# Optimization experiments

Hardware: AMD Instinct MI355X
Metric: run time of the kernel (lower is better)

## Reference

```python
import jax, jax.numpy as jnp
import numpy as np

N, M, D_IN, HID = 6144, 6144, 16, 256
TEMP = 0.1


def setup_inputs() -> dict:
    key = jax.random.key(0)
    ks = jax.random.split(key, 6)
    sc = lambda k, shape, s: jax.random.normal(k, shape, jnp.float32) * s
    return {
        "q_multivectors": jax.random.normal(ks[0], (N, D_IN), jnp.float32),
        "ret_multivectors": jax.random.normal(ks[1], (M, D_IN), jnp.float32),
        # compressor: LazyLinear(D_IN->HID), GELU, Linear(HID->HID)
        "W1": sc(ks[2], (HID, D_IN), 0.1), "b1": jnp.zeros((HID,), jnp.float32),
        "W2": sc(ks[3], (HID, HID), 0.05), "b2": jnp.zeros((HID,), jnp.float32),
        # nn.Bilinear(HID, HID, 1): weight [1,HID,HID] -> [HID,HID], bias [1] -> scalar
        "Wb": sc(ks[4], (HID, HID), 0.02), "b_bil": jnp.zeros((), jnp.float32),
        "slack_q": jnp.zeros((1,), jnp.float32),
        "slack_ret": jnp.zeros((1,), jnp.float32),
    }


def reference(q_multivectors, ret_multivectors, W1, b1, W2, b2, Wb, b_bil, slack_q, slack_ret):
    def compress(x):  # Linear -> exact GELU -> Linear
        return jax.nn.gelu(x @ W1.T + b1, approximate=False) @ W2.T + b2

    h_q = compress(q_multivectors)    # [n, H]
    h_r = compress(ret_multivectors)  # [m, H]

    # Bilinear(h_q_i, h_r_j) as low-rank factorization: (h_q @ Wb) @ h_r^T + bias
    logits = (h_q @ Wb) @ h_r.T + b_bil  # [n, m]
    n, m = logits.shape

    # row softmax with slack column, then drop slack
    with_slack_col = jnp.concatenate([logits, jnp.broadcast_to(slack_q, (n, 1))], axis=1)
    pi_rows = jax.nn.softmax(with_slack_col / TEMP, axis=1)[:, :-1]

    # column softmax with slack row, then drop slack
    with_slack_row = jnp.concatenate([logits, jnp.broadcast_to(slack_ret, (1, m))], axis=0)
    pi_cols = jax.nn.softmax(with_slack_row / TEMP, axis=0)[:-1, :]

    pi_approx = 0.5 * (pi_rows + pi_cols)
    return pi_approx, logits
```

## Files before the change

kernel.cpp:

```cpp
#include <hip/hip_runtime.h>
#include <hip/hip_bf16.h>
#include <math.h>

#define NQ 6144
#define MR 6144
#define DIN 16
#define HID 256
#define INV_T 10.0f

typedef __attribute__((ext_vector_type(4))) float f32x4;
typedef __attribute__((ext_vector_type(8))) short bf16x8;


static __device__ __forceinline__ unsigned short f2bf(float f) {
  __hip_bfloat16 h = __float2bfloat16(f);
  return __builtin_bit_cast(unsigned short, h);
}

static __device__ __forceinline__ void gload16(const void* g, void* l) {
  __builtin_amdgcn_global_load_lds(
      (const __attribute__((address_space(1))) unsigned int*)g,
      (__attribute__((address_space(3))) unsigned int*)l, 16, 0, 0);
}

__global__ __launch_bounds__(256) void k_prep(
    const float* __restrict__ W2, const float* __restrict__ Wb,
    unsigned short* __restrict__ W2bf, unsigned short* __restrict__ Wbt)
{
  const int idx = blockIdx.x * 256 + threadIdx.x;
  W2bf[idx] = f2bf(W2[idx]);
  const int j = idx >> 8, c = idx & 255;
  Wbt[(size_t)c * 256 + j] = f2bf(Wb[idx]);
}

__global__ __launch_bounds__(256) void k_compress(
    const float* __restrict__ q, const float* __restrict__ ret,
    const float* __restrict__ W1, const float* __restrict__ b1,
    const unsigned short* __restrict__ W2bf, const float* __restrict__ b2,
    const unsigned short* __restrict__ Wbt,
    unsigned short* __restrict__ Apk, unsigned short* __restrict__ Bpk)
{
  const int tid = threadIdx.x;
  const bool is_q = blockIdx.x < (NQ / 16);
  const int grp = is_q ? blockIdx.x : blockIdx.x - NQ / 16;
  const int row0 = grp * 16;
  const float* x = is_q ? q : ret;

  __shared__ float xs[16][DIN];
  __shared__ __align__(16) unsigned short tb[16 * 256];
  __shared__ __align__(16) unsigned short hb[16 * 256];

  ((float*)xs)[tid] = x[(size_t)row0 * DIN + tid];
  __syncthreads();

  {
    float w[DIN];
#pragma unroll
    for (int d = 0; d < DIN; ++d) w[d] = W1[tid * DIN + d];
    const float bb = b1[tid];
#pragma unroll
    for (int rr = 0; rr < 16; ++rr) {
      float a = bb;
#pragma unroll
      for (int d = 0; d < DIN; ++d) a += xs[rr][d] * w[d];
      a = 0.5f * a * (1.0f + erff(a * 0.70710678118654752f));
      tb[rr * 256 + (tid ^ ((rr & 7) << 3))] = f2bf(a);
    }
  }
  __syncthreads();

  const int wid = tid >> 6, lane = tid & 63;
  const int l15 = lane & 15;
  const int lk = (lane >> 4) * 8;

  {
    f32x4 acc[4];
#pragma unroll
    for (int ci = 0; ci < 4; ++ci) acc[ci] = (f32x4)0.0f;

    for (int kk = 0; kk < HID; kk += 32) {
      const bf16x8 a = *(const bf16x8*)&tb[l15 * 256 + ((kk + lk) ^ ((l15 & 7) << 3))];
#pragma unroll
      for (int ci = 0; ci < 4; ++ci) {
        const int bc = wid * 64 + ci * 16 + l15;
        const bf16x8 b = *(const bf16x8*)&W2bf[(size_t)bc * HID + kk + lk];
        acc[ci] = __builtin_amdgcn_mfma_f32_16x16x32_bf16(a, b, acc[ci], 0, 0, 0);
      }
    }

#pragma unroll
    for (int ci = 0; ci < 4; ++ci) {
      const int col = wid * 64 + ci * 16 + l15;
      const float bb2 = b2[col];
#pragma unroll
      for (int qq = 0; qq < 4; ++qq) {
        const int row = (lane >> 4) * 4 + qq;
        hb[row * 256 + (col ^ ((row & 7) << 3))] = f2bf(acc[ci][qq] + bb2);
      }
    }
  }
  __syncthreads();

  if (!is_q) {
#pragma unroll
    for (int i = 0; i < 2; ++i) {
      const int u = i * 256 + tid;
      const int kc = u >> 6, lr = (u >> 2) & 15, ks = u & 3;
      const int k = kc * 32 + ks * 8;
      const bf16x8 v = *(const bf16x8*)&hb[lr * 256 + (k ^ ((lr & 7) << 3))];
      *(bf16x8*)&Bpk[(size_t)grp * 4096 + (size_t)u * 8] = v;
    }
    return;
  }

  {
    f32x4 acc[4];
#pragma unroll
    for (int ci = 0; ci < 4; ++ci) acc[ci] = (f32x4)0.0f;

    for (int kk = 0; kk < HID; kk += 32) {
      const bf16x8 a = *(const bf16x8*)&hb[l15 * 256 + ((kk + lk) ^ ((l15 & 7) << 3))];
#pragma unroll
      for (int ci = 0; ci < 4; ++ci) {
        const int bc = wid * 64 + ci * 16 + l15;
        const bf16x8 b = *(const bf16x8*)&Wbt[(size_t)bc * HID + kk + lk];
        acc[ci] = __builtin_amdgcn_mfma_f32_16x16x32_bf16(a, b, acc[ci], 0, 0, 0);
      }
    }

#pragma unroll
    for (int ci = 0; ci < 4; ++ci) {
      const int col = wid * 64 + ci * 16 + l15;
#pragma unroll
      for (int qq = 0; qq < 4; ++qq) {
        const int row = (lane >> 4) * 4 + qq;
        tb[row * 256 + (col ^ ((row & 7) << 3))] = f2bf(acc[ci][qq]);
      }
    }
  }
  __syncthreads();

#pragma unroll
  for (int i = 0; i < 2; ++i) {
    const int u = i * 256 + tid;
    const int kc = u >> 6, lr = (u >> 2) & 15, ks = u & 3;
    const int k = kc * 32 + ks * 8;
    const bf16x8 v = *(const bf16x8*)&tb[lr * 256 + (k ^ ((lr & 7) << 3))];
    *(bf16x8*)&Apk[(size_t)grp * 4096 + (size_t)u * 8] = v;
  }
}

__global__ __launch_bounds__(512, 4) void k_gemm(
    const unsigned short* __restrict__ Apk,
    const unsigned short* __restrict__ Bpk,
    const float* __restrict__ b_bil,
    float* __restrict__ logF,
    float* __restrict__ rowPS,
    float* __restrict__ colPS)
{
  const int tid = threadIdx.x;
  const int wid = tid >> 6, lane = tid & 63;
  const int wr = wid >> 1, wc = wid & 1;

  const int orig = blockIdx.y * 48 + blockIdx.x;
  const int nid = (orig & 7) * 144 + (orig >> 3);
  const int brow = (nid / 48) * 256;
  const int bcol = (nid % 48) * 128;
  const int brow16 = brow >> 4, bcol16 = bcol >> 4;

  __shared__ __align__(16) unsigned short As[2][8192];
  __shared__ __align__(16) unsigned short Bs[2][4096];

  const int l15 = lane & 15;
  const int ksg = lane >> 4;

  f32x4 acc[4][4];
#pragma unroll
  for (int i = 0; i < 4; ++i)
#pragma unroll
    for (int j = 0; j < 4; ++j) acc[i][j] = (f32x4)0.0f;

  gload16(Apk + (size_t)(brow16 + 2 * wid) * 4096 + lane * 8,
          &As[0][(2 * wid) * 512]);
  gload16(Apk + (size_t)(brow16 + 2 * wid + 1) * 4096 + lane * 8,
          &As[0][(2 * wid + 1) * 512]);
  gload16(Bpk + (size_t)(bcol16 + wid) * 4096 + lane * 8, &Bs[0][wid * 512]);

  int cur = 0;
  for (int kc = 0; kc < 8; ++kc) {
    __syncthreads();
    if (kc < 7) {
      const int kn = (kc + 1) * 512;
      gload16(Apk + (size_t)(brow16 + 2 * wid) * 4096 + kn + lane * 8,
              &As[cur ^ 1][(2 * wid) * 512]);
      gload16(Apk + (size_t)(brow16 + 2 * wid + 1) * 4096 + kn + lane * 8,
              &As[cur ^ 1][(2 * wid + 1) * 512]);
      gload16(Bpk + (size_t)(bcol16 + wid) * 4096 + kn + lane * 8,
              &Bs[cur ^ 1][wid * 512]);
    }
    const int fo = l15 * 32 + ksg * 8;
    bf16x8 a[4], b[4];
#pragma unroll
    for (int mi = 0; mi < 4; ++mi)
      a[mi] = *(const bf16x8*)&As[cur][(wr * 4 + mi) * 512 + fo];
#pragma unroll
    for (int ni = 0; ni < 4; ++ni)
      b[ni] = *(const bf16x8*)&Bs[cur][(wc * 4 + ni) * 512 + fo];
#pragma unroll
    for (int mi = 0; mi < 4; ++mi)
#pragma unroll
      for (int ni = 0; ni < 4; ++ni)
        acc[mi][ni] = __builtin_amdgcn_mfma_f32_16x16x32_bf16(
            a[mi], b[ni], acc[mi][ni], 0, 0, 0);
    cur ^= 1;
  }

  const float bb = b_bil[0];
#pragma unroll
  for (int mi = 0; mi < 4; ++mi)
#pragma unroll
    for (int ni = 0; ni < 4; ++ni)
#pragma unroll
      for (int qq = 0; qq < 4; ++qq) acc[mi][ni][qq] += bb;

  const int r0 = brow + wr * 64 + ksg * 4;
  const int c0 = bcol + wc * 64 + l15;
#pragma unroll
  for (int mi = 0; mi < 4; ++mi)
#pragma unroll
    for (int qq = 0; qq < 4; ++qq) {
      const int rr = r0 + mi * 16 + qq;
#pragma unroll
      for (int ni = 0; ni < 4; ++ni)
        logF[(size_t)rr * MR + c0 + ni * 16] = acc[mi][ni][qq];
    }

  const int cb = (bcol >> 6) + wc;
  const int rb = (brow >> 6) + wr;
  float csum[4] = {0.0f, 0.0f, 0.0f, 0.0f};
#pragma unroll
  for (int mi = 0; mi < 4; ++mi) {
#pragma unroll
    for (int qq = 0; qq < 4; ++qq) {
      float rsum = 0.0f;
#pragma unroll
      for (int ni = 0; ni < 4; ++ni) {
        const float e = __expf(acc[mi][ni][qq] * INV_T);
        rsum += e;
        csum[ni] += e;
      }
      rsum += __shfl_xor(rsum, 1);
      rsum += __shfl_xor(rsum, 2);
      rsum += __shfl_xor(rsum, 4);
      rsum += __shfl_xor(rsum, 8);
      if (l15 == 0) rowPS[(size_t)cb * NQ + (r0 + mi * 16 + qq)] = rsum;
    }
  }
#pragma unroll
  for (int ni = 0; ni < 4; ++ni) {
    csum[ni] += __shfl_xor(csum[ni], 16);
    csum[ni] += __shfl_xor(csum[ni], 32);
  }
  if (lane < 16) {
#pragma unroll
    for (int ni = 0; ni < 4; ++ni)
      colPS[(size_t)rb * MR + (bcol + wc * 64 + ni * 16 + lane)] = csum[ni];
  }
}

__global__ __launch_bounds__(256) void k_comb(
    const float* __restrict__ rowPS, const float* __restrict__ colPS,
    const float* __restrict__ slack_q, const float* __restrict__ slack_ret,
    float* __restrict__ rowR, float* __restrict__ colR)
{
  const int idx = blockIdx.x * 256 + threadIdx.x;
  const bool is_row = idx < NQ;
  const int i = is_row ? idx : idx - NQ;
  const float* ps = is_row ? rowPS : colPS;

  float s = 0.0f;
  for (int c = 0; c < 96; ++c) s += ps[(size_t)c * NQ + i];
  s += __expf((is_row ? slack_q[0] : slack_ret[0]) * INV_T);

  if (is_row) rowR[i] = 0.5f / s;
  else        colR[i] = 0.5f / s;
}

__global__ __launch_bounds__(256) void k_final(
    const float* __restrict__ logF,
    const float* __restrict__ rowR, const float* __restrict__ colR,
    float* __restrict__ out_pi)
{
  const int row = blockIdx.x / 6;
  const int seg = blockIdx.x % 6;
  const int col = seg * 1024 + threadIdx.x * 4;
  const size_t base = (size_t)row * MR + col;

  const float rinv = rowR[row];
  const f32x4 cv = *(const f32x4*)(colR + col);
  const f32x4 l4 = *(const f32x4*)(logF + base);

  f32x4 o;
  o.x = __expf(l4.x * INV_T) * (rinv + cv.x);
  o.y = __expf(l4.y * INV_T) * (rinv + cv.y);
  o.z = __expf(l4.z * INV_T) * (rinv + cv.z);
  o.w = __expf(l4.w * INV_T) * (rinv + cv.w);
  __builtin_nontemporal_store(o, (f32x4*)(out_pi + base));
}

extern "C" void kernel_launch(void* const* d_in, const int* in_sizes, int n_in,
                              void* d_out, int out_size, void* d_ws, size_t ws_size,
                              hipStream_t stream) {
  const float* q  = (const float*)d_in[0];
  const float* r  = (const float*)d_in[1];
  const float* W1 = (const float*)d_in[2];
  const float* b1 = (const float*)d_in[3];
  const float* W2 = (const float*)d_in[4];
  const float* b2 = (const float*)d_in[5];
  const float* Wb = (const float*)d_in[6];
  const float* bb = (const float*)d_in[7];
  const float* sq = (const float*)d_in[8];
  const float* sr = (const float*)d_in[9];

  float* out_pi = (float*)d_out;
  float* out_lg = out_pi + (size_t)NQ * MR;

  char* w = (char*)d_ws;
  size_t off = 0;
  auto alloc = [&](size_t bytes) {
    void* p = w + off;
    off += (bytes + 255) & ~(size_t)255;
    return p;
  };
  unsigned short* Apk  = (unsigned short*)alloc((size_t)NQ * HID * 2);
  unsigned short* Bpk  = (unsigned short*)alloc((size_t)MR * HID * 2);
  unsigned short* W2bf = (unsigned short*)alloc((size_t)HID * HID * 2);
  unsigned short* Wbt  = (unsigned short*)alloc((size_t)HID * HID * 2);
  float* rowR = (float*)alloc((size_t)NQ * 4);
  float* colR = (float*)alloc((size_t)MR * 4);

  float* rowPS = out_pi + (size_t)0 * 96 * NQ;
  float* colPS = out_pi + (size_t)1 * 96 * NQ;

  k_prep<<<dim3(HID * HID / 256), 256, 0, stream>>>(W2, Wb, W2bf, Wbt);
  k_compress<<<dim3((NQ + MR) / 16), 256, 0, stream>>>(q, r, W1, b1, W2bf, b2,
                                                       Wbt, Apk, Bpk);
  k_gemm<<<dim3(48, 24), 512, 0, stream>>>(Apk, Bpk, bb, out_lg, rowPS, colPS);
  k_comb<<<dim3((NQ + MR) / 256), 256, 0, stream>>>(
      rowPS, colPS, sq, sr, rowR, colR);
  k_final<<<dim3(NQ * 6), 256, 0, stream>>>(out_lg, rowR, colR, out_pi);
}
```

Before: 128.0 us.

## Replace partial-sum buffers and combine kernel with atomic reductions

The GEMM epilogue now accumulates row and column exp sums directly into global arrays with atomicAdd instead of writing per-tile partial sums. This removes the separate combine kernel and its 96-way strided reads. The zeroing moves into the prep kernel, and the final kernel folds in the slack and reciprocal while processing 8 elements per thread. The block-to-XCD mapping also changes to 2D tiles per XCD for better L2 reuse. In exchange it adds atomic contention and makes the summation order nondeterministic.

```diff
diff --git a/kernel.cpp b/kernel.cpp
--- a/kernel.cpp
+++ b/kernel.cpp
@@ -25,12 +25,15 @@
 
 __global__ __launch_bounds__(256) void k_prep(
     const float* __restrict__ W2, const float* __restrict__ Wb,
-    unsigned short* __restrict__ W2bf, unsigned short* __restrict__ Wbt)
+    unsigned short* __restrict__ W2bf, unsigned short* __restrict__ Wbt,
+    float* __restrict__ rowS, float* __restrict__ colS)
 {
   const int idx = blockIdx.x * 256 + threadIdx.x;
   W2bf[idx] = f2bf(W2[idx]);
   const int j = idx >> 8, c = idx & 255;
   Wbt[(size_t)c * 256 + j] = f2bf(Wb[idx]);
+  if (idx < NQ) rowS[idx] = 0.0f;
+  else if (idx < NQ + MR) colS[idx - NQ] = 0.0f;
 }
 
 __global__ __launch_bounds__(256) void k_compress(
@@ -155,17 +158,19 @@
     const unsigned short* __restrict__ Bpk,
     const float* __restrict__ b_bil,
     float* __restrict__ logF,
-    float* __restrict__ rowPS,
-    float* __restrict__ colPS)
+    float* __restrict__ rowS,
+    float* __restrict__ colS)
 {
   const int tid = threadIdx.x;
   const int wid = tid >> 6, lane = tid & 63;
   const int wr = wid >> 1, wc = wid & 1;
 
   const int orig = blockIdx.y * 48 + blockIdx.x;
-  const int nid = (orig & 7) * 144 + (orig >> 3);
-  const int brow = (nid / 48) * 256;
-  const int bcol = (nid % 48) * 128;
+  const int xcd = orig & 7;
+  const int idx = orig >> 3;
+  const int rr_ = idx / 12, cc_ = idx % 12;
+  const int brow = ((xcd >> 2) * 12 + rr_) * 256;
+  const int bcol = ((xcd & 3) * 12 + cc_) * 128;
   const int brow16 = brow >> 4, bcol16 = bcol >> 4;
 
   __shared__ __align__(16) unsigned short As[2][8192];
@@ -235,8 +240,6 @@
         logF[(size_t)rr * MR + c0 + ni * 16] = acc[mi][ni][qq];
     }
 
-  const int cb = (bcol >> 6) + wc;
-  const int rb = (brow >> 6) + wr;
   float csum[4] = {0.0f, 0.0f, 0.0f, 0.0f};
 #pragma unroll
   for (int mi = 0; mi < 4; ++mi) {
@@ -253,7 +256,7 @@
       rsum += __shfl_xor(rsum, 2);
       rsum += __shfl_xor(rsum, 4);
       rsum += __shfl_xor(rsum, 8);
-      if (l15 == 0) rowPS[(size_t)cb * NQ + (r0 + mi * 16 + qq)] = rsum;
+      if (l15 == 0) atomicAdd(&rowS[r0 + mi * 16 + qq], rsum);
     }
   }
 #pragma unroll
@@ -264,48 +267,41 @@
   if (lane < 16) {
 #pragma unroll
     for (int ni = 0; ni < 4; ++ni)
-      colPS[(size_t)rb * MR + (bcol + wc * 64 + ni * 16 + lane)] = csum[ni];
-  }
-}
-
-__global__ __launch_bounds__(256) void k_comb(
-    const float* __restrict__ rowPS, const float* __restrict__ colPS,
-    const float* __restrict__ slack_q, const float* __restrict__ slack_ret,
-    float* __restrict__ rowR, float* __restrict__ colR)
-{
-  const int idx = blockIdx.x * 256 + threadIdx.x;
-  const bool is_row = idx < NQ;
-  const int i = is_row ? idx : idx - NQ;
-  const float* ps = is_row ? rowPS : colPS;
-
-  float s = 0.0f;
-  for (int c = 0; c < 96; ++c) s += ps[(size_t)c * NQ + i];
-  s += __expf((is_row ? slack_q[0] : slack_ret[0]) * INV_T);
-
-  if (is_row) rowR[i] = 0.5f / s;
-  else        colR[i] = 0.5f / s;
+      atomicAdd(&colS[bcol + wc * 64 + ni * 16 + lane], csum[ni]);
+  }
 }
 
 __global__ __launch_bounds__(256) void k_final(
     const float* __restrict__ logF,
-    const float* __restrict__ rowR, const float* __restrict__ colR,
+    const float* __restrict__ rowS, const float* __restrict__ colS,
+    const float* __restrict__ slack_q, const float* __restrict__ slack_ret,
     float* __restrict__ out_pi)
 {
-  const int row = blockIdx.x / 6;
-  const int seg = blockIdx.x % 6;
-  const int col = seg * 1024 + threadIdx.x * 4;
+  const int row = blockIdx.x / 3;
+  const int seg = blockIdx.x % 3;
+  const int col = seg * 2048 + threadIdx.x * 8;
   const size_t base = (size_t)row * MR + col;
 
-  const float rinv = rowR[row];
-  const f32x4 cv = *(const f32x4*)(colR + col);
-  const f32x4 l4 = *(const f32x4*)(logF + base);
-
-  f32x4 o;
-  o.x = __expf(l4.x * INV_T) * (rinv + cv.x);
-  o.y = __expf(l4.y * INV_T) * (rinv + cv.y);
-  o.z = __expf(l4.z * INV_T) * (rinv + cv.z);
-  o.w = __expf(l4.w * INV_T) * (rinv + cv.w);
-  __builtin_nontemporal_store(o, (f32x4*)(out_pi + base));
+  const float esq = __expf(slack_q[0] * INV_T);
+  const float esr = __expf(slack_ret[0] * INV_T);
+  const float rinv = 0.5f / (rowS[row] + esq);
+
+  const f32x4 cs0 = *(const f32x4*)(colS + col);
+  const f32x4 cs1 = *(const f32x4*)(colS + col + 4);
+  const f32x4 l0 = *(const f32x4*)(logF + base);
+  const f32x4 l1 = *(const f32x4*)(logF + base + 4);
+
+  f32x4 o0, o1;
+  o0.x = __expf(l0.x * INV_T) * (rinv + 0.5f / (cs0.x + esr));
+  o0.y = __expf(l0.y * INV_T) * (rinv + 0.5f / (cs0.y + esr));
+  o0.z = __expf(l0.z * INV_T) * (rinv + 0.5f / (cs0.z + esr));
+  o0.w = __expf(l0.w * INV_T) * (rinv + 0.5f / (cs0.w + esr));
+  o1.x = __expf(l1.x * INV_T) * (rinv + 0.5f / (cs1.x + esr));
+  o1.y = __expf(l1.y * INV_T) * (rinv + 0.5f / (cs1.y + esr));
+  o1.z = __expf(l1.z * INV_T) * (rinv + 0.5f / (cs1.z + esr));
+  o1.w = __expf(l1.w * INV_T) * (rinv + 0.5f / (cs1.w + esr));
+  __builtin_nontemporal_store(o0, (f32x4*)(out_pi + base));
+  __builtin_nontemporal_store(o1, (f32x4*)(out_pi + base + 4));
 }
 
 extern "C" void kernel_launch(void* const* d_in, const int* in_sizes, int n_in,
@@ -336,17 +332,14 @@
   unsigned short* Bpk  = (unsigned short*)alloc((size_t)MR * HID * 2);
   unsigned short* W2bf = (unsigned short*)alloc((size_t)HID * HID * 2);
   unsigned short* Wbt  = (unsigned short*)alloc((size_t)HID * HID * 2);
-  float* rowR = (float*)alloc((size_t)NQ * 4);
-  float* colR = (float*)alloc((size_t)MR * 4);
-
-  float* rowPS = out_pi + (size_t)0 * 96 * NQ;
-  float* colPS = out_pi + (size_t)1 * 96 * NQ;
-
-  k_prep<<<dim3(HID * HID / 256), 256, 0, stream>>>(W2, Wb, W2bf, Wbt);
+  float* rowS = (float*)alloc((size_t)NQ * 4);
+  float* colS = (float*)alloc((size_t)MR * 4);
+
+  k_prep<<<dim3(HID * HID / 256), 256, 0, stream>>>(W2, Wb, W2bf, Wbt,
+                                                    rowS, colS);
   k_compress<<<dim3((NQ + MR) / 16), 256, 0, stream>>>(q, r, W1, b1, W2bf, b2,
                                                        Wbt, Apk, Bpk);
-  k_gemm<<<dim3(48, 24), 512, 0, stream>>>(Apk, Bpk, bb, out_lg, rowPS, colPS);
-  k_comb<<<dim3((NQ + MR) / 256), 256, 0, stream>>>(
-      rowPS, colPS, sq, sr, rowR, colR);
-  k_final<<<dim3(NQ * 6), 256, 0, stream>>>(out_lg, rowR, colR, out_pi);
-}
+  k_gemm<<<dim3(48, 24), 512, 0, stream>>>(Apk, Bpk, bb, out_lg, rowS, colS);
+  k_final<<<dim3(NQ * 3), 256, 0, stream>>>(out_lg, rowS, colS, sq, sr,
+                                            out_pi);
+}
```

New measurement: 137.3 us. 7.3% more time.

## Shrink GEMM block tile to 128x128 and load K in two large halves

Applied to the files above, without the earlier changes.

The logits GEMM moves from 512-thread blocks computing 256x128 tiles to 256-thread blocks computing 128x128 tiles, which doubles the grid to 48x48. The per-chunk double-buffered K pipeline is replaced by two stages that each load half of K (four chunks) into a larger LDS buffer, followed by four MFMA steps. The intent is more independent blocks to hide latency and fewer barriers per block. The cost is lost load/compute overlap inside a block, more global reads of the packed operands overall, and higher LDS use per block, which limits occupancy.

```diff
diff --git a/kernel.cpp b/kernel.cpp
--- a/kernel.cpp
+++ b/kernel.cpp
@@ -150,7 +150,7 @@
   }
 }
 
-__global__ __launch_bounds__(512, 4) void k_gemm(
+__global__ __launch_bounds__(256) void k_gemm(
     const unsigned short* __restrict__ Apk,
     const unsigned short* __restrict__ Bpk,
     const float* __restrict__ b_bil,
@@ -163,13 +163,13 @@
   const int wr = wid >> 1, wc = wid & 1;
 
   const int orig = blockIdx.y * 48 + blockIdx.x;
-  const int nid = (orig & 7) * 144 + (orig >> 3);
-  const int brow = (nid / 48) * 256;
+  const int nid = (orig & 7) * 288 + (orig >> 3);
+  const int brow = (nid / 48) * 128;
   const int bcol = (nid % 48) * 128;
   const int brow16 = brow >> 4, bcol16 = bcol >> 4;
 
-  __shared__ __align__(16) unsigned short As[2][8192];
-  __shared__ __align__(16) unsigned short Bs[2][4096];
+  __shared__ __align__(16) unsigned short As[8 * 4 * 512];
+  __shared__ __align__(16) unsigned short Bs[8 * 4 * 512];
 
   const int l15 = lane & 15;
   const int ksg = lane >> 4;
@@ -180,39 +180,39 @@
 #pragma unroll
     for (int j = 0; j < 4; ++j) acc[i][j] = (f32x4)0.0f;
 
-  gload16(Apk + (size_t)(brow16 + 2 * wid) * 4096 + lane * 8,
-          &As[0][(2 * wid) * 512]);
-  gload16(Apk + (size_t)(brow16 + 2 * wid + 1) * 4096 + lane * 8,
-          &As[0][(2 * wid + 1) * 512]);
-  gload16(Bpk + (size_t)(bcol16 + wid) * 4096 + lane * 8, &Bs[0][wid * 512]);
-
-  int cur = 0;
-  for (int kc = 0; kc < 8; ++kc) {
+#pragma unroll
+  for (int h = 0; h < 2; ++h) {
+    if (h == 1) __syncthreads();
+#pragma unroll
+    for (int g2 = 0; g2 < 2; ++g2) {
+      const int g = 2 * wid + g2;
+      const size_t asrc = (size_t)(brow16 + g) * 4096 + h * 2048 + lane * 8;
+      const size_t bsrc = (size_t)(bcol16 + g) * 4096 + h * 2048 + lane * 8;
+#pragma unroll
+      for (int kci = 0; kci < 4; ++kci) {
+        gload16(Apk + asrc + kci * 512, &As[(g * 4 + kci) * 512]);
+        gload16(Bpk + bsrc + kci * 512, &Bs[(g * 4 + kci) * 512]);
+      }
+    }
     __syncthreads();
-    if (kc < 7) {
-      const int kn = (kc + 1) * 512;
-      gload16(Apk + (size_t)(brow16 + 2 * wid) * 4096 + kn + lane * 8,
-              &As[cur ^ 1][(2 * wid) * 512]);
-      gload16(Apk + (size_t)(brow16 + 2 * wid + 1) * 4096 + kn + lane * 8,
-              &As[cur ^ 1][(2 * wid + 1) * 512]);
-      gload16(Bpk + (size_t)(bcol16 + wid) * 4096 + kn + lane * 8,
-              &Bs[cur ^ 1][wid * 512]);
-    }
-    const int fo = l15 * 32 + ksg * 8;
-    bf16x8 a[4], b[4];
-#pragma unroll
-    for (int mi = 0; mi < 4; ++mi)
-      a[mi] = *(const bf16x8*)&As[cur][(wr * 4 + mi) * 512 + fo];
-#pragma unroll
-    for (int ni = 0; ni < 4; ++ni)
-      b[ni] = *(const bf16x8*)&Bs[cur][(wc * 4 + ni) * 512 + fo];
-#pragma unroll
-    for (int mi = 0; mi < 4; ++mi)
+
+#pragma unroll
+    for (int kci = 0; kci < 4; ++kci) {
+      const int fo = l15 * 32 + ksg * 8;
+      bf16x8 a[4], b[4];
+#pragma unroll
+      for (int mi = 0; mi < 4; ++mi)
+        a[mi] = *(const bf16x8*)&As[((wr * 4 + mi) * 4 + kci) * 512 + fo];
 #pragma unroll
       for (int ni = 0; ni < 4; ++ni)
-        acc[mi][ni] = __builtin_amdgcn_mfma_f32_16x16x32_bf16(
-            a[mi], b[ni], acc[mi][ni], 0, 0, 0);
-    cur ^= 1;
+        b[ni] = *(const bf16x8*)&Bs[((wc * 4 + ni) * 4 + kci) * 512 + fo];
+#pragma unroll
+      for (int mi = 0; mi < 4; ++mi)
+#pragma unroll
+        for (int ni = 0; ni < 4; ++ni)
+          acc[mi][ni] = __builtin_amdgcn_mfma_f32_16x16x32_bf16(
+              a[mi], b[ni], acc[mi][ni], 0, 0, 0);
+    }
   }
 
   const float bb = b_bil[0];
@@ -345,7 +345,7 @@
   k_prep<<<dim3(HID * HID / 256), 256, 0, stream>>>(W2, Wb, W2bf, Wbt);
   k_compress<<<dim3((NQ + MR) / 16), 256, 0, stream>>>(q, r, W1, b1, W2bf, b2,
                                                        Wbt, Apk, Bpk);
-  k_gemm<<<dim3(48, 24), 512, 0, stream>>>(Apk, Bpk, bb, out_lg, rowPS, colPS);
+  k_gemm<<<dim3(48, 48), 256, 0, stream>>>(Apk, Bpk, bb, out_lg, rowPS, colPS);
   k_comb<<<dim3((NQ + MR) / 256), 256, 0, stream>>>(
       rowPS, colPS, sq, sr, rowR, colR);
   k_final<<<dim3(NQ * 6), 256, 0, stream>>>(out_lg, rowR, colR, out_pi);
```

Result: slower. 138.4 us (+8.2%).
